# Optimization experiments

Measured on AMD Instinct MI355X. Metric: run time of the kernel, lower is better.

The kernel has to match this reference:

```python
import jax, jax.numpy as jnp
import numpy as np
from jax import lax

N, T, D, W, H, V = 256, 64, 1280, 256, 512, 10000
NULL_IDX = 0  # ignore_index


def setup_inputs() -> dict:
    key = jax.random.key(0)
    ks = jax.random.split(key, 9)
    features = jax.random.normal(ks[0], (N, D), dtype=jnp.float32)
    captions = jax.random.randint(ks[1], (N, T + 1), 0, V, dtype=jnp.int64)
    # learned parameters
    W_proj = jax.random.normal(ks[2], (D, H), dtype=jnp.float32) / np.sqrt(D)
    b_proj = jnp.zeros((H,), dtype=jnp.float32)
    W_embed = jax.random.normal(ks[3], (V, W), dtype=jnp.float32) / np.sqrt(V)
    Wx = jax.random.normal(ks[4], (W, H), dtype=jnp.float32) / np.sqrt(W)
    Wh = jax.random.normal(ks[5], (H, H), dtype=jnp.float32) / np.sqrt(H)
    b = jnp.zeros((H,), dtype=jnp.float32)
    W_out = jax.random.normal(ks[6], (H, V), dtype=jnp.float32) / np.sqrt(H)
    b_out = jnp.zeros((V,), dtype=jnp.float32)
    return {"features": features, "captions": captions, "W_proj": W_proj,
            "b_proj": b_proj, "W_embed": W_embed, "Wx": Wx, "Wh": Wh, "b": b,
            "W_out": W_out, "b_out": b_out}


def reference(features, captions, W_proj, b_proj, W_embed, Wx, Wh, b, W_out, b_out):
    captions_in = captions[:, :-1]   # (N, T)
    captions_out = captions[:, 1:]   # (N, T)

    h0 = features @ W_proj + b_proj                      # (N, H)
    x = W_embed[captions_in]                             # (N, T, W)
    # Precompute input-to-hidden part; recurrence only needs h @ Wh.
    xWxb = jnp.einsum('ntw,wh->nth', x, Wx) + b          # (N, T, H)

    def step(h_prev, xt):
        h_next = jnp.tanh(h_prev @ Wh + xt)
        return h_next, h_next

    _, hs = lax.scan(step, h0, jnp.swapaxes(xWxb, 0, 1))  # (T, N, H)
    h = jnp.swapaxes(hs, 0, 1)                            # (N, T, H)

    scores = jnp.einsum('nth,hv->ntv', h, W_out) + b_out  # (N, T, V)
    logp = jax.nn.log_softmax(scores, axis=-1)
    nll = -jnp.take_along_axis(logp, captions_out[..., None], axis=-1)[..., 0]
    mask = (captions_out != NULL_IDX).astype(nll.dtype)
    loss = jnp.sum(nll * mask) / N
    return loss
```

## Files before the change

### kernel.cpp

```cpp
#include <hip/hip_runtime.h>
#include <hip/hip_bf16.h>
#include <hip/hip_fp8.h>

#define NB 256
#define TT 64
#define DD 1280
#define WW 256
#define HH 512
#define VV 10000
#define VP 10112
#define NCT 79
#define MROWS (NB*TT)

typedef short short8 __attribute__((ext_vector_type(8)));
typedef float f32x4 __attribute__((ext_vector_type(4)));
typedef int   int4v __attribute__((ext_vector_type(4)));
typedef int   int8v __attribute__((ext_vector_type(8)));

static __device__ __forceinline__ unsigned short f2bf(float x){
    unsigned int u = __float_as_uint(x);
    unsigned int r = u + 0x7FFFu + ((u >> 16) & 1u);
    return (unsigned short)(r >> 16);
}
static __device__ __forceinline__ float bf2f(unsigned short u){
    return __uint_as_float(((unsigned int)u) << 16);
}
static __device__ __forceinline__ unsigned char f2f8(float x){
    __hip_fp8_e4m3 q(x);
    return (unsigned char)q.__x;
}
static __device__ __forceinline__ unsigned enc4(float x){
    unsigned s = (x < 0.f) ? 8u : 0u;
    float a = fabsf(x);
    unsigned m;
    if      (a < 0.25f) m = 0;
    else if (a < 0.75f) m = 1;
    else if (a < 1.25f) m = 2;
    else if (a < 1.75f) m = 3;
    else if (a < 2.5f)  m = 4;
    else if (a < 3.5f)  m = 5;
    else if (a < 5.0f)  m = 6;
    else                m = 7;
    return s | m;
}
static __device__ __forceinline__ void gload16b(const unsigned char* g, unsigned char* l){
    __builtin_amdgcn_global_load_lds(
        (const __attribute__((address_space(1))) void*)g,
        (__attribute__((address_space(3))) void*)l, 16, 0, 0);
}


__global__ __launch_bounds__(256) void k_prep(const float* __restrict__ W_proj,
                                              unsigned short* __restrict__ Wpb,
                                              const float* __restrict__ Wx,
                                              unsigned short* __restrict__ WxT,
                                              const float* __restrict__ Wh,
                                              unsigned char* __restrict__ WhT4,
                                              const float* __restrict__ W_out,
                                              unsigned char* __restrict__ WoT8p,
                                              const float* __restrict__ bo,
                                              float* __restrict__ bop){
    __shared__ unsigned short tileS[64][17];
    int b = blockIdx.x;
    int tid = threadIdx.x;
    if (b < 640){
        int i = b*256 + tid;
        float4 f = *reinterpret_cast<const float4*>(W_proj + (size_t)i*4);
        unsigned short* o = Wpb + (size_t)i*4;
        o[0]=f2bf(f.x); o[1]=f2bf(f.y); o[2]=f2bf(f.z); o[3]=f2bf(f.w);
    } else if (b < 768){
        int r = b - 640;
        int c0 = (r & 7)*64, r0 = (r >> 3)*16;
        int c = tid & 63, rr = tid >> 6;
        #pragma unroll
        for (int j = 0; j < 4; ++j){
            int rw_ = rr + j*4;
            tileS[c][rw_] = f2bf(Wx[(size_t)(r0+rw_)*HH + c0 + c]);
        }
        __syncthreads();
        int rw = tid & 15, cw = tid >> 4;
        #pragma unroll
        for (int j = 0; j < 4; ++j){
            int c2 = cw + j*16;
            WxT[(size_t)(c0+c2)*WW + r0 + rw] = tileS[c2][rw];
        }
    } else if (b < 1280){
        int r = b - 768;
        int j = r >> 1;
        int col = (r & 1)*256 + tid;
        float w0 = Wh[(size_t)(2*j  )*HH + col] * 32.0f;
        float w1 = Wh[(size_t)(2*j+1)*HH + col] * 32.0f;
        WhT4[(size_t)col*256 + j] = (unsigned char)(enc4(w0) | (enc4(w1) << 4));
    } else if (b < 6336){
        unsigned char (*tileC)[20] = reinterpret_cast<unsigned char (*)[20]>(&tileS[0][0]);
        int r = b - 1280;
        int c0 = (r % 158)*64, r0 = (r / 158)*16;
        int c = tid & 63, rr = tid >> 6;
        #pragma unroll
        for (int j = 0; j < 4; ++j){
            int rw_ = rr + j*4;
            unsigned char v = 0;
            if (c0 + c < VV) v = f2f8(W_out[(size_t)(r0+rw_)*VV + c0 + c]);
            tileC[c][rw_] = v;
        }
        __syncthreads();
        int rw = tid & 15, cw = tid >> 4;
        #pragma unroll
        for (int j = 0; j < 4; ++j){
            int c2 = cw + j*16;
            int col = c0 + c2, k = r0 + rw;
            if (col < VP){
                size_t addr = ((size_t)((col >> 7)*4 + (k >> 7)))*16384
                            + (unsigned)((col & 127)*128 + (k & 127));
                WoT8p[addr] = tileC[c2][rw];
            }
        }
    } else {
        int i = (b - 6336)*256 + tid;
        if (i < VP) bop[i] = (i < VV) ? bo[i] : -30000.0f;
    }
}

__global__ __launch_bounds__(512) void k_h0(const float* __restrict__ feat,
                                            const unsigned short* __restrict__ Wpb,
                                            const float* __restrict__ bp,
                                            float* __restrict__ h0){
    int n0 = blockIdx.x*2;
    int h = threadIdx.x;
    const float* f0 = feat + (size_t)(n0+0)*DD;
    const float* f1 = feat + (size_t)(n0+1)*DD;
    float a0=0.f, a1=0.f;
    for (int d = 0; d < DD; d += 4){
        #pragma unroll
        for (int j = 0; j < 4; ++j){
            float w = bf2f(Wpb[(size_t)(d+j)*HH + h]);
            a0 += f0[d+j]*w;
            a1 += f1[d+j]*w;
        }
    }
    float bb = bp[h];
    h0[(size_t)(n0+0)*HH+h] = a0+bb;
    h0[(size_t)(n0+1)*HH+h] = a1+bb;
}

__global__ __launch_bounds__(256) void k_e2(const float* __restrict__ We,
                                            const unsigned short* __restrict__ WxT,
                                            const float* __restrict__ bias,
                                            unsigned short* __restrict__ E2b){
    int lane = threadIdx.x & 63;
    int wv   = threadIdx.x >> 6;
    int l15 = lane & 15, lhi = lane >> 4;
    int rbase = blockIdx.x*64 + wv*16;
    int arow = rbase + l15; if (arow > VV-1) arow = VV-1;
    short8 a[8];
    #pragma unroll
    for (int kk = 0; kk < 8; ++kk){
        const float* src = We + (size_t)arow*WW + kk*32 + lhi*8;
        float4 g0 = *reinterpret_cast<const float4*>(src);
        float4 g1 = *reinterpret_cast<const float4*>(src + 4);
        short8 v;
        v[0]=(short)f2bf(g0.x); v[1]=(short)f2bf(g0.y); v[2]=(short)f2bf(g0.z); v[3]=(short)f2bf(g0.w);
        v[4]=(short)f2bf(g1.x); v[5]=(short)f2bf(g1.y); v[6]=(short)f2bf(g1.z); v[7]=(short)f2bf(g1.w);
        a[kk] = v;
    }
    int ct0 = blockIdx.y*16;
    for (int ct = ct0; ct < ct0+16; ++ct){
        int c0 = ct*16;
        f32x4 acc = {0.f,0.f,0.f,0.f};
        #pragma unroll
        for (int kk = 0; kk < 8; ++kk){
            short8 b = *reinterpret_cast<const short8*>(WxT + (size_t)(c0 + l15)*WW + kk*32 + lhi*8);
            acc = __builtin_amdgcn_mfma_f32_16x16x32_bf16(a[kk], b, acc, 0, 0, 0);
        }
        float bb = bias[c0 + l15];
        #pragma unroll
        for (int r = 0; r < 4; ++r){
            int row = rbase + lhi*4 + r;
            if (row < VV) E2b[(size_t)row*HH + c0 + l15] = f2bf(acc[r] + bb);
        }
    }
}

__global__ __launch_bounds__(512, 2) void k_rnn(const float* __restrict__ h0,
                                                const unsigned char* __restrict__ WhT4,
                                                const unsigned short* __restrict__ E2b,
                                                const int* __restrict__ caps,
                                                unsigned char* __restrict__ hA8){
    __shared__ __align__(32) unsigned char hl[2][HH];
    int tid = threadIdx.x;
    int lane = tid & 63, wv = tid >> 6;
    int l15 = lane & 15, lhi = lane >> 4;
    int n = blockIdx.x;
    int c0w = wv*64;
    int mycol = c0w + lane;
    unsigned char* hbase = hA8 + ((size_t)((n>>1)*4 + (wv>>1)))*16384
                               + (unsigned)((n&1)*64*128 + (mycol & 127));

    int4v b[4][4];
    #pragma unroll
    for (int ct = 0; ct < 4; ++ct){
        int col = c0w + ct*16 + l15;
        #pragma unroll
        for (int kt = 0; kt < 4; ++kt){
            b[ct][kt] = *reinterpret_cast<const int4v*>(WhT4 + (size_t)col*256 + kt*64 + lhi*16);
            asm volatile("" : "+v"(b[ct][kt]));
        }
    }
    hl[0][tid] = f2f8(h0[(size_t)n*HH + tid]);
    __syncthreads();
    int cur = 0;
    for (int t = 0; t < TT; ++t){
        int tok = caps[n*(TT+1) + t];
        unsigned short xv = E2b[(size_t)tok*HH + mycol];
        int8v a[4];
        #pragma unroll
        for (int kt = 0; kt < 4; ++kt)
            a[kt] = *reinterpret_cast<const int8v*>(&hl[cur][kt*128 + lhi*32]);
        f32x4 acc[4];
        #pragma unroll
        for (int ct = 0; ct < 4; ++ct){
            acc[ct] = (f32x4){0.f,0.f,0.f,0.f};
            #pragma unroll
            for (int kt = 0; kt < 4; ++kt){
                int8v bb = __builtin_shufflevector(b[ct][kt], b[ct][kt], 0,1,2,3,0,1,2,3);
                acc[ct] = __builtin_amdgcn_mfma_scale_f32_16x16x128_f8f6f4(
                    a[kt], bb, acc[ct],
                    0, 4,
                    0, (int)0x7F7F7F7F,
                    0, (int)0x7A7A7A7A);
            }
        }
        float v = (lhi == 0) ? acc[0][0] : (lhi == 1) ? acc[1][0]
                : (lhi == 2) ? acc[2][0] : acc[3][0];
        float x = v + bf2f(xv);
        float e = __expf(2.f*x);
        float th = 1.f - 2.f/(e + 1.f);
        unsigned char hv = f2f8(th);
        hl[cur^1][mycol] = hv;
        hbase[t*128] = hv;
        __syncthreads();
        cur ^= 1;
    }
}

__global__ __launch_bounds__(512) void k_scores(const unsigned char* __restrict__ hA8,
                                                const unsigned char* __restrict__ WoT8p,
                                                const float* __restrict__ bop,
                                                const int* __restrict__ caps,
                                                float* __restrict__ pps,
                                                float* __restrict__ pts){
    __shared__ unsigned char As[16384];
    __shared__ unsigned char Bs[16384];
    int bid = blockIdx.x;
    int x = bid & 7;
    int local = bid >> 3;
    int ct = local >> 4;
    int rt = x*16 + (local & 15);

    int tid = threadIdx.x;
    int lane = tid & 63, wv = tid >> 6;
    int l15 = lane & 15, lhi = lane >> 4;
    int wr = wv >> 1, wc = wv & 1;
    const unsigned char* Abase = hA8   + (size_t)rt*65536;
    const unsigned char* Bbase = WoT8p + (size_t)ct*65536;

    unsigned coff[2];
    #pragma unroll
    for (int i = 0; i < 2; ++i){
        unsigned chunk = (unsigned)(i*512 + tid);
        unsigned rowloc = chunk >> 3;
        coff[i] = rowloc*128 + (((chunk & 7u) ^ (rowloc & 7u))*16u);
    }

    f32x4 acc[2][4];
    #pragma unroll
    for (int m = 0; m < 2; ++m)
        #pragma unroll
        for (int n = 0; n < 4; ++n)
            acc[m][n] = (f32x4){0.f,0.f,0.f,0.f};

    for (int kt = 0; kt < 4; ++kt){
        #pragma unroll
        for (int i = 0; i < 2; ++i){
            gload16b(Abase + kt*16384 + coff[i], As + (unsigned)((i*512 + tid - lane + lane) * 16));
            gload16b(Bbase + kt*16384 + coff[i], Bs + (unsigned)((i*512 + tid) * 16));
        }
        __syncthreads();
        int8v af[2];
        #pragma unroll
        for (int m = 0; m < 2; ++m){
            unsigned row = (unsigned)(wr*32 + m*16 + l15);
            int4v c0 = *reinterpret_cast<const int4v*>(As + row*128 + (((unsigned)(lhi*2+0) ^ (row&7))*16));
            int4v c1 = *reinterpret_cast<const int4v*>(As + row*128 + (((unsigned)(lhi*2+1) ^ (row&7))*16));
            af[m] = __builtin_shufflevector(c0, c1, 0,1,2,3,4,5,6,7);
        }
        #pragma unroll
        for (int n = 0; n < 4; ++n){
            unsigned col = (unsigned)(wc*64 + n*16 + l15);
            int4v c0 = *reinterpret_cast<const int4v*>(Bs + col*128 + (((unsigned)(lhi*2+0) ^ (col&7))*16));
            int4v c1 = *reinterpret_cast<const int4v*>(Bs + col*128 + (((unsigned)(lhi*2+1) ^ (col&7))*16));
            int8v bf = __builtin_shufflevector(c0, c1, 0,1,2,3,4,5,6,7);
            #pragma unroll
            for (int m = 0; m < 2; ++m)
                acc[m][n] = __builtin_amdgcn_mfma_scale_f32_16x16x128_f8f6f4(
                    af[m], bf, acc[m][n],
                    0, 0,
                    0, (int)0x7F7F7F7F,
                    0, (int)0x7F7F7F7F);
        }
        __syncthreads();
    }

    int tg[2][4];
    float srun[2][4], ts[2][4];
    #pragma unroll
    for (int m = 0; m < 2; ++m)
        #pragma unroll
        for (int r = 0; r < 4; ++r){
            int gr = rt*128 + wr*32 + m*16 + lhi*4 + r;
            tg[m][r] = caps[(gr >> 6)*(TT+1) + (gr & 63) + 1];
            srun[m][r] = 0.f; ts[m][r] = 0.f;
        }
    #pragma unroll
    for (int n = 0; n < 4; ++n){
        int colg = ct*128 + wc*64 + n*16 + l15;
        float bb = bop[colg];
        #pragma unroll
        for (int m = 0; m < 2; ++m)
            #pragma unroll
            for (int r = 0; r < 4; ++r){
                float sc = acc[m][n][r] + bb;
                srun[m][r] += __expf(sc);
                if (tg[m][r] == colg) ts[m][r] += sc;
            }
    }
    #pragma unroll
    for (int off = 1; off < 16; off <<= 1)
        #pragma unroll
        for (int m = 0; m < 2; ++m)
            #pragma unroll
            for (int r = 0; r < 4; ++r){
                srun[m][r] += __shfl_xor(srun[m][r], off, 64);
                ts[m][r]   += __shfl_xor(ts[m][r],   off, 64);
            }
    float* red = (float*)As;
    if (wc == 1 && l15 == 0){
        #pragma unroll
        for (int m = 0; m < 2; ++m)
            #pragma unroll
            for (int r = 0; r < 4; ++r){
                int ri = wr*32 + m*16 + lhi*4 + r;
                red[ri]       = srun[m][r];
                red[128 + ri] = ts[m][r];
            }
    }
    __syncthreads();
    if (wc == 0 && l15 == 0){
        #pragma unroll
        for (int m = 0; m < 2; ++m)
            #pragma unroll
            for (int r = 0; r < 4; ++r){
                int ri = wr*32 + m*16 + lhi*4 + r;
                int gr = rt*128 + ri;
                pps[(size_t)ct*MROWS + gr] = srun[m][r] + red[ri];
                pts[(size_t)ct*MROWS + gr] = ts[m][r]   + red[128 + ri];
            }
    }
}

__global__ __launch_bounds__(256) void k_loss1(const float* __restrict__ pps,
                                               const float* __restrict__ pts,
                                               const int* __restrict__ caps,
                                               float* __restrict__ bsum){
    __shared__ float reds[256], redt[256];
    int tid = threadIdx.x;
    int rloc = tid & 63, q = tid >> 6;
    int row = blockIdx.x*64 + rloc;
    int c0 = q*20, c1 = (q == 3) ? NCT : c0 + 20;
    float s = 0.f, t0 = 0.f;
    for (int ct = c0; ct < c1; ++ct){
        s  += pps[(size_t)ct*MROWS + row];
        t0 += pts[(size_t)ct*MROWS + row];
    }
    reds[tid] = s; redt[tid] = t0;
    __syncthreads();
    if (q == 0){
        s  = reds[rloc] + reds[64+rloc] + reds[128+rloc] + reds[192+rloc];
        t0 = redt[rloc] + redt[64+rloc] + redt[128+rloc] + redt[192+rloc];
        int tgt = caps[(row >> 6)*(TT+1) + (row & 63) + 1];
        reds[rloc] = (tgt != 0) ? (__logf(s) - t0) : 0.f;
    }
    __syncthreads();
    if (tid < 32) reds[tid] += reds[tid+32];
    __syncthreads();
    if (tid < 16) reds[tid] += reds[tid+16];
    __syncthreads();
    if (tid < 8)  reds[tid] += reds[tid+8];
    __syncthreads();
    if (tid < 4)  reds[tid] += reds[tid+4];
    __syncthreads();
    if (tid == 0) bsum[blockIdx.x] = reds[0] + reds[1] + reds[2] + reds[3];
}

__global__ __launch_bounds__(64) void k_loss2(const float* __restrict__ bsum, float* __restrict__ out){
    __shared__ float red[64];
    int tid = threadIdx.x;
    red[tid] = bsum[tid] + bsum[tid+64] + bsum[tid+128] + bsum[tid+192];
    __syncthreads();
    for (int off = 32; off > 0; off >>= 1){
        if (tid < off) red[tid] += red[tid+off];
        __syncthreads();
    }
    if (tid == 0) out[0] = red[0] / (float)NB;
}

extern "C" void kernel_launch(void* const* d_in, const int* in_sizes, int n_in,
                              void* d_out, int out_size, void* d_ws, size_t ws_size,
                              hipStream_t stream) {
    const float* features = (const float*)d_in[0];
    const int*   captions = (const int*)  d_in[1];
    const float* W_proj   = (const float*)d_in[2];
    const float* b_proj   = (const float*)d_in[3];
    const float* W_embed  = (const float*)d_in[4];
    const float* Wx       = (const float*)d_in[5];
    const float* Wh       = (const float*)d_in[6];
    const float* b_       = (const float*)d_in[7];
    const float* W_out    = (const float*)d_in[8];
    const float* b_out    = (const float*)d_in[9];
    float* out = (float*)d_out;

    char* ws = (char*)d_ws;
    unsigned short* E2b   = (unsigned short*)(ws + 0);
    float*          h0    = (float*)         (ws + 10240000);
    unsigned char*  WhT4  = (unsigned char*) (ws + 10764288);
    unsigned short* WxT   = (unsigned short*)(ws + 10895360);
    unsigned char*  WoT8p = (unsigned char*) (ws + 11157504);
    float*          bop   = (float*)         (ws + 16334848);
    unsigned char*  hA8   = (unsigned char*) (ws + 16375296);
    float*          pps   = (float*)         (ws + 24763904);
    float*          pts   = (float*)         (ws + 29941248);
    float*          bsum  = (float*)         (ws + 35118592);
    unsigned short* Wpb   = (unsigned short*)(ws + 35119616);
    if (ws_size < 36430336u) return;

    k_prep<<<6376, 256, 0, stream>>>(W_proj, Wpb, Wx, WxT, Wh, WhT4, W_out, WoT8p, b_out, bop);
    k_h0<<<NB/2, 512, 0, stream>>>(features, Wpb, b_proj, h0);
    k_e2<<<dim3(157,2), 256, 0, stream>>>(W_embed, WxT, b_, E2b);
    k_rnn<<<NB, 512, 0, stream>>>(h0, WhT4, E2b, captions, hA8);
    k_scores<<<128*NCT, 512, 0, stream>>>(hA8, WoT8p, bop, captions, pps, pts);
    k_loss1<<<256, 256, 0, stream>>>(pps, pts, captions, bsum);
    k_loss2<<<1, 64, 0, stream>>>(bsum, out);
}
```

Before: 323.0 us.

## Move target-logit gather out of scores GEMM epilogue into a separate dot kernel

The scores kernel no longer loads captions or tracks the target logit per column tile. It now only accumulates exp-sums, using exp2 with log2e folded into the bias and an fma. A new small kernel computes each row's target logit directly as an fp8 dot product of h with the target's W_out column, so the pts array of 79 partial sums and its reads in loss1 go away. This trims epilogue registers and compares plus global traffic, at the cost of an extra kernel launch and a separate target-score computation that must match the GEMM's numerics.

```diff
diff --git a/kernel.cpp b/kernel.cpp
--- a/kernel.cpp
+++ b/kernel.cpp
@@ -28,6 +28,10 @@
 static __device__ __forceinline__ unsigned char f2f8(float x){
     __hip_fp8_e4m3 q(x);
     return (unsigned char)q.__x;
+}
+static __device__ __forceinline__ float f82f(unsigned char b){
+    __hip_fp8_e4m3 q; q.__x = b;
+    return (float)q;
 }
 static __device__ __forceinline__ unsigned enc4(float x){
     unsigned s = (x < 0.f) ? 8u : 0u;
@@ -117,7 +121,7 @@
         }
     } else {
         int i = (b - 6336)*256 + tid;
-        if (i < VP) bop[i] = (i < VV) ? bo[i] : -30000.0f;
+        if (i < VP) bop[i] = (i < VV) ? bo[i]*1.44269504f : -30000.0f;
     }
 }
 
@@ -246,9 +250,7 @@
 __global__ __launch_bounds__(512) void k_scores(const unsigned char* __restrict__ hA8,
                                                 const unsigned char* __restrict__ WoT8p,
                                                 const float* __restrict__ bop,
-                                                const int* __restrict__ caps,
-                                                float* __restrict__ pps,
-                                                float* __restrict__ pts){
+                                                float* __restrict__ pps){
     __shared__ unsigned char As[16384];
     __shared__ unsigned char Bs[16384];
     int bid = blockIdx.x;
@@ -282,7 +284,7 @@
     for (int kt = 0; kt < 4; ++kt){
         #pragma unroll
         for (int i = 0; i < 2; ++i){
-            gload16b(Abase + kt*16384 + coff[i], As + (unsigned)((i*512 + tid - lane + lane) * 16));
+            gload16b(Abase + kt*16384 + coff[i], As + (unsigned)((i*512 + tid) * 16));
             gload16b(Bbase + kt*16384 + coff[i], Bs + (unsigned)((i*512 + tid) * 16));
         }
         __syncthreads();
@@ -311,38 +313,29 @@
         __syncthreads();
     }
 
-    int tg[2][4];
-    float srun[2][4], ts[2][4];
+    const float LOG2E = 1.44269504f;
+    float srun[2][4];
     #pragma unroll
     for (int m = 0; m < 2; ++m)
         #pragma unroll
-        for (int r = 0; r < 4; ++r){
-            int gr = rt*128 + wr*32 + m*16 + lhi*4 + r;
-            tg[m][r] = caps[(gr >> 6)*(TT+1) + (gr & 63) + 1];
-            srun[m][r] = 0.f; ts[m][r] = 0.f;
-        }
+        for (int r = 0; r < 4; ++r) srun[m][r] = 0.f;
     #pragma unroll
     for (int n = 0; n < 4; ++n){
         int colg = ct*128 + wc*64 + n*16 + l15;
-        float bb = bop[colg];
+        float bb2 = bop[colg];
         #pragma unroll
         for (int m = 0; m < 2; ++m)
             #pragma unroll
-            for (int r = 0; r < 4; ++r){
-                float sc = acc[m][n][r] + bb;
-                srun[m][r] += __expf(sc);
-                if (tg[m][r] == colg) ts[m][r] += sc;
-            }
+            for (int r = 0; r < 4; ++r)
+                srun[m][r] += exp2f(fmaf(acc[m][n][r], LOG2E, bb2));
     }
     #pragma unroll
     for (int off = 1; off < 16; off <<= 1)
         #pragma unroll
         for (int m = 0; m < 2; ++m)
             #pragma unroll
-            for (int r = 0; r < 4; ++r){
+            for (int r = 0; r < 4; ++r)
                 srun[m][r] += __shfl_xor(srun[m][r], off, 64);
-                ts[m][r]   += __shfl_xor(ts[m][r],   off, 64);
-            }
     float* red = (float*)As;
     if (wc == 1 && l15 == 0){
         #pragma unroll
@@ -350,8 +343,7 @@
             #pragma unroll
             for (int r = 0; r < 4; ++r){
                 int ri = wr*32 + m*16 + lhi*4 + r;
-                red[ri]       = srun[m][r];
-                red[128 + ri] = ts[m][r];
+                red[ri] = srun[m][r];
             }
     }
     __syncthreads();
@@ -363,32 +355,52 @@
                 int ri = wr*32 + m*16 + lhi*4 + r;
                 int gr = rt*128 + ri;
                 pps[(size_t)ct*MROWS + gr] = srun[m][r] + red[ri];
-                pts[(size_t)ct*MROWS + gr] = ts[m][r]   + red[128 + ri];
             }
     }
 }
 
+__global__ __launch_bounds__(256) void k_tsc(const unsigned char* __restrict__ hA8,
+                                             const unsigned char* __restrict__ WoT8p,
+                                             const float* __restrict__ bo,
+                                             const int* __restrict__ caps,
+                                             float* __restrict__ t0arr){
+    int lane = threadIdx.x & 63, w = threadIdx.x >> 6;
+    int row = blockIdx.x*4 + w;
+    int tgt = caps[(row >> 6)*(TT+1) + (row & 63) + 1];
+    int k0 = lane*8;
+    int ktile = k0 >> 7, kin = k0 & 127;
+    const unsigned char* hp = hA8   + ((size_t)((row >> 7)*4 + ktile))*16384
+                                    + (unsigned)((row & 127)*128 + kin);
+    const unsigned char* wp = WoT8p + ((size_t)((tgt >> 7)*4 + ktile))*16384
+                                    + (unsigned)((tgt & 127)*128 + kin);
+    float sum = 0.f;
+    #pragma unroll
+    for (int j = 0; j < 8; ++j)
+        sum += f82f(hp[j]) * f82f(wp[j]);
+    #pragma unroll
+    for (int off = 1; off < 64; off <<= 1)
+        sum += __shfl_xor(sum, off, 64);
+    if (lane == 0) t0arr[row] = sum + bo[tgt];
+}
+
 __global__ __launch_bounds__(256) void k_loss1(const float* __restrict__ pps,
-                                               const float* __restrict__ pts,
+                                               const float* __restrict__ t0arr,
                                                const int* __restrict__ caps,
                                                float* __restrict__ bsum){
-    __shared__ float reds[256], redt[256];
+    __shared__ float reds[256];
     int tid = threadIdx.x;
     int rloc = tid & 63, q = tid >> 6;
     int row = blockIdx.x*64 + rloc;
     int c0 = q*20, c1 = (q == 3) ? NCT : c0 + 20;
-    float s = 0.f, t0 = 0.f;
-    for (int ct = c0; ct < c1; ++ct){
-        s  += pps[(size_t)ct*MROWS + row];
-        t0 += pts[(size_t)ct*MROWS + row];
-    }
-    reds[tid] = s; redt[tid] = t0;
+    float s = 0.f;
+    for (int ct = c0; ct < c1; ++ct)
+        s += pps[(size_t)ct*MROWS + row];
+    reds[tid] = s;
     __syncthreads();
     if (q == 0){
-        s  = reds[rloc] + reds[64+rloc] + reds[128+rloc] + reds[192+rloc];
-        t0 = redt[rloc] + redt[64+rloc] + redt[128+rloc] + redt[192+rloc];
+        s = reds[rloc] + reds[64+rloc] + reds[128+rloc] + reds[192+rloc];
         int tgt = caps[(row >> 6)*(TT+1) + (row & 63) + 1];
-        reds[rloc] = (tgt != 0) ? (__logf(s) - t0) : 0.f;
+        reds[rloc] = (tgt != 0) ? (__logf(s) - t0arr[row]) : 0.f;
     }
     __syncthreads();
     if (tid < 32) reds[tid] += reds[tid+32];
@@ -438,16 +450,17 @@
     float*          bop   = (float*)         (ws + 16334848);
     unsigned char*  hA8   = (unsigned char*) (ws + 16375296);
     float*          pps   = (float*)         (ws + 24763904);
-    float*          pts   = (float*)         (ws + 29941248);
-    float*          bsum  = (float*)         (ws + 35118592);
-    unsigned short* Wpb   = (unsigned short*)(ws + 35119616);
-    if (ws_size < 36430336u) return;
+    float*          t0arr = (float*)         (ws + 29941248);
+    float*          bsum  = (float*)         (ws + 30006784);
+    unsigned short* Wpb   = (unsigned short*)(ws + 30007808);
+    if (ws_size < 31318528u) return;
 
     k_prep<<<6376, 256, 0, stream>>>(W_proj, Wpb, Wx, WxT, Wh, WhT4, W_out, WoT8p, b_out, bop);
     k_h0<<<NB/2, 512, 0, stream>>>(features, Wpb, b_proj, h0);
     k_e2<<<dim3(157,2), 256, 0, stream>>>(W_embed, WxT, b_, E2b);
     k_rnn<<<NB, 512, 0, stream>>>(h0, WhT4, E2b, captions, hA8);
-    k_scores<<<128*NCT, 512, 0, stream>>>(hA8, WoT8p, bop, captions, pps, pts);
-    k_loss1<<<256, 256, 0, stream>>>(pps, pts, captions, bsum);
+    k_scores<<<128*NCT, 512, 0, stream>>>(hA8, WoT8p, bop, pps);
+    k_tsc<<<MROWS/4, 256, 0, stream>>>(hA8, WoT8p, b_out, captions, t0arr);
+    k_loss1<<<256, 256, 0, stream>>>(pps, t0arr, captions, bsum);
     k_loss2<<<1, 64, 0, stream>>>(bsum, out);
 }
```

Result: faster. 302.2 us (-6.4%).
